# Kernel optimization log

Measured on AMD Instinct MI355X. Metric: run time of the kernel, lower is better.

## Reference

```python
import jax, jax.numpy as jnp
import numpy as np

G = 2            # num_codevector_groups
C = 320          # num_codevectors_per_group
VQ_DIM = 256     # codevector_dim
HID = 512        # conv_dimensions[-1]
TAU = 2.0


def setup_inputs() -> dict:
    key = jax.random.key(0)
    k1, k2, k3, k4 = jax.random.split(key, 4)
    B, S = 16, 2048
    x = jax.random.normal(k1, (B, S, HID), dtype=jnp.float32)
    # iid Gumbel(0,1) noise, same shape as flattened logits [B*S*G, C]
    u = jax.random.uniform(k2, (B * S * G, C), dtype=jnp.float32, minval=1e-6, maxval=1.0 - 1e-6)
    gumbel = -jnp.log(-jnp.log(u))
    Wq = jax.random.normal(k3, (G * C, HID), dtype=jnp.float32) * (1.0 / np.sqrt(HID))
    bq = jnp.zeros((G * C,), dtype=jnp.float32)
    codevectors = jax.random.uniform(k4, (1, G * C, VQ_DIM // G), dtype=jnp.float32)
    return {"x": x, "gumbel": gumbel, "Wq": Wq, "bq": bq, "codevectors": codevectors}


def reference(x, gumbel, Wq, bq, codevectors):
    B, S, H = x.shape
    N = B * S
    logits = jnp.einsum('bsh,gh->bsg', x, Wq) + bq          # [B, S, G*C]
    logits = logits.reshape(N * G, C)

    # hard gumbel-softmax (training path) with straight-through estimator
    y_soft = jax.nn.softmax((logits + gumbel) / TAU, axis=-1)
    idx = jnp.argmax(y_soft, axis=-1)
    y_hard = jax.nn.one_hot(idx, C, dtype=y_soft.dtype)
    probs = y_hard + y_soft - jax.lax.stop_gradient(y_soft)  # [N*G, C]

    # perplexity from plain softmax of logits (no gumbel noise), masked_token_idx=None
    soft_probs = jax.nn.softmax(logits.reshape(N, G, C), axis=-1)
    mean_p = soft_probs.mean(axis=0)                          # [G, C]
    perplexity = jnp.exp(-jnp.sum(mean_p * jnp.log(mean_p + 1e-7), axis=-1)).sum()

    # weighted sum over codes per group == einsum (same math as broadcast*sum in torch)
    cv = codevectors.reshape(G, C, VQ_DIM // G)               # [G, C, d]
    sel = jnp.einsum('ngc,gcd->ngd', probs.reshape(N, G, C), cv)
    selected_codes = sel.reshape(B, S, VQ_DIM)
    return selected_codes, perplexity
```

## Files before the change

### kernel.cpp

```cpp
#include <hip/hip_runtime.h>
#include <hip/hip_fp16.h>

#define HID 512
#define GC  640
#define CC  320
#define GG  2
#define DHALF 128
#define MARGIN 0.004f
#define FB 4

typedef __attribute__((ext_vector_type(8))) _Float16 half8;
typedef __attribute__((ext_vector_type(4))) float float4v;

__device__ __forceinline__ void gload16(const void* g, void* l) {
    __builtin_amdgcn_global_load_lds(
        (const __attribute__((address_space(1))) void*)(unsigned long long)g,
        (__attribute__((address_space(3))) void*)(unsigned)(unsigned long long)l,
        16, 0, 0);
}

__global__ __launch_bounds__(256) void zero_misc(float* meanAcc, int* cnt) {
    for (int i = threadIdx.x; i < GC; i += 256) meanAcc[i] = 0.f;
    if (threadIdx.x < 2) cnt[threadIdx.x] = 0;
}

__global__ __launch_bounds__(256) void convert_f16(
    const float* __restrict__ in, unsigned short* __restrict__ out, int n8)
{
    int i = blockIdx.x * 256 + threadIdx.x;
    if (i >= n8) return;
    const float4* p = (const float4*)in + (size_t)i * 2;
    float4 v0 = p[0], v1 = p[1];
    float f[8] = {v0.x, v0.y, v0.z, v0.w, v1.x, v1.y, v1.z, v1.w};
    unsigned r[4];
#pragma unroll
    for (int j = 0; j < 4; ++j) {
        __half2 hh = __float22half2_rn(make_float2(f[2*j], f[2*j+1]));
        r[j] = __builtin_bit_cast(unsigned, hh);
    }
    uint4 o = {r[0], r[1], r[2], r[3]};
    *(uint4*)(out + (size_t)i * 8) = o;
}

__global__ __launch_bounds__(512, 4) void fused(
    const float* __restrict__ X, const unsigned short* __restrict__ Wh,
    const float* __restrict__ bq, const float* __restrict__ gum,
    const float* __restrict__ cv, float* __restrict__ out,
    float* __restrict__ meanAcc, int* __restrict__ cnt,
    int* __restrict__ flags0, int* __restrict__ flags1)
{
    __shared__ __align__(16) unsigned short As[128 * 32];
    __shared__ __align__(16) unsigned short Bs[384 * 32];
    __shared__ float bqs[CC];
    __shared__ float smean[CC];

    const int tid  = threadIdx.x;
    const int lane = tid & 63;
    const int wid  = tid >> 6;
    const int lq   = lane & 15;
    const int q    = lane >> 4;

    int bid = blockIdx.x;
    int nwg = gridDim.x;
    int swz = ((nwg & 7) == 0) ? (bid & 7) * (nwg >> 3) + (bid >> 3) : bid;
    const int g    = swz & 1;
    const int tok0 = (swz >> 1) * 128;
    int* flagsg = g ? flags1 : flags0;

    for (int i = tid; i < CC; i += 512) { bqs[i] = bq[g * CC + i]; smean[i] = 0.f; }

    float4v acc[20];
#pragma unroll
    for (int j = 0; j < 20; ++j) acc[j] = (float4v){0.f, 0.f, 0.f, 0.f};

    const int arow = tid >> 2, aslot = tid & 3;
    const float* xsrc = X + (size_t)(tok0 + arow) * HID + aslot * 8;

    for (int k0 = 0; k0 < HID; k0 += 32) {
        float4 xa = *(const float4*)(xsrc + k0);
        float4 xb = *(const float4*)(xsrc + k0 + 4);
        half8 h;
        h[0] = (_Float16)xa.x; h[1] = (_Float16)xa.y;
        h[2] = (_Float16)xa.z; h[3] = (_Float16)xa.w;
        h[4] = (_Float16)xb.x; h[5] = (_Float16)xb.y;
        h[6] = (_Float16)xb.z; h[7] = (_Float16)xb.w;
        *(half8*)&As[arow * 32 + aslot * 8] = h;
#pragma unroll
        for (int ii = 0; ii < 3; ++ii) {
            const int iss = wid * 3 + ii;
            int e  = iss * 64 + lane;
            int br = e >> 2; if (br > 319) br = 319;
            int bs = e & 3;
            gload16(Wh + ((size_t)(g * CC + br)) * HID + k0 + bs * 8,
                    &Bs[iss * 512]);
        }
        __syncthreads();
        half8 a = *(const half8*)&As[(wid * 16 + lq) * 32 + q * 8];
#pragma unroll
        for (int j = 0; j < 20; ++j) {
            half8 b = *(const half8*)&Bs[(j * 16 + lq) * 32 + q * 8];
            acc[j] = __builtin_amdgcn_mfma_f32_16x16x32_f16(a, b, acc[j], 0, 0, 0);
        }
        __syncthreads();
    }

    float macc[20];
#pragma unroll
    for (int j = 0; j < 20; ++j) macc[j] = 0.f;

#pragma unroll
    for (int r = 0; r < 4; ++r) {
        const int rowL  = wid * 16 + q * 4 + r;
        const int tglob = tok0 + rowL;
        const float* grow = gum + ((size_t)tglob * GG + g) * CC;
        float le[20];
        float s = 0.f;
        float b = -3.0e38f; int bi = 0; float s2 = -3.0e38f;
#pragma unroll
        for (int j = 0; j < 20; ++j) {
            const int c = j * 16 + lq;
            float lg = acc[j][r] + bqs[c];
            float v  = lg + grow[c];
            if (v > b)       { s2 = b; b = v; bi = c; }
            else if (v > s2) { s2 = v; }
            le[j] = __expf(lg); s += le[j];
        }
#pragma unroll
        for (int m = 1; m < 16; m <<= 1) {
            float os  = __shfl_xor(s,  m, 64);
            float ob  = __shfl_xor(b,  m, 64);
            int   obi = __shfl_xor(bi, m, 64);
            float os2 = __shfl_xor(s2, m, 64);
            s += os;
            if (ob > b || (ob == b && obi < bi)) { s2 = fmaxf(os2, b); b = ob; bi = obi; }
            else                                 { s2 = fmaxf(s2, ob); }
        }
        float inv = 1.f / s;
#pragma unroll
        for (int j = 0; j < 20; ++j) macc[j] += le[j] * inv;

        if (lq == 0 && (b - s2) < MARGIN) {
            int p = atomicAdd(&cnt[g], 1);
            flagsg[p] = tglob;
        }
        const float* cvp = cv + ((size_t)(g * CC + bi)) * DHALF + lq * 8;
        float4 c0v = *(const float4*)cvp;
        float4 c1v = *(const float4*)(cvp + 4);
        float* op = out + (size_t)tglob * 256 + g * DHALF + lq * 8;
        *(float4*)op       = c0v;
        *(float4*)(op + 4) = c1v;
    }
#pragma unroll
    for (int j = 0; j < 20; ++j) {
        macc[j] += __shfl_xor(macc[j], 16, 64);
        macc[j] += __shfl_xor(macc[j], 32, 64);
    }
    if (lane < 16) {
#pragma unroll
        for (int j = 0; j < 20; ++j)
            atomicAdd(&smean[j * 16 + lq], macc[j]);
    }
    __syncthreads();
    for (int i = tid; i < CC; i += 512)
        atomicAdd(&meanAcc[g * CC + i], smean[i]);
}

__global__ __launch_bounds__(320) void fixup(
    const float* __restrict__ X, const float* __restrict__ W,
    const float* __restrict__ bq, const float* __restrict__ gum,
    const float* __restrict__ cv, float* __restrict__ out,
    const int* __restrict__ flags0, const int* __restrict__ flags1,
    const int* __restrict__ cnt)
{
    __shared__ float xs[FB][HID];
    __shared__ float vals[FB][CC];
    __shared__ int stok[FB];
    const int tid = threadIdx.x;
    const int n0 = cnt[0], n1 = cnt[1];
    const int nb0 = (n0 + FB - 1) / FB;
    const int nb1 = (n1 + FB - 1) / FB;

    for (int bb = blockIdx.x; bb < nb0 + nb1; bb += gridDim.x) {
        const int g    = (bb < nb0) ? 0 : 1;
        const int lb   = (bb < nb0) ? bb : bb - nb0;
        const int n    = g ? n1 : n0;
        const int* fl  = g ? flags1 : flags0;
        const int r0   = lb * FB;
        const int nr   = (n - r0 < FB) ? (n - r0) : FB;

        if (tid < FB) {
            int idx = r0 + tid;
            if (idx >= n) idx = n - 1;
            stok[tid] = fl[idx];
        }
        __syncthreads();
        for (int i = tid; i < FB * (HID / 4); i += 320) {
            int r = i >> 7, k4 = i & 127;
            *(float4*)&xs[r][k4 * 4] = *(const float4*)(X + (size_t)stok[r] * HID + k4 * 4);
        }
        __syncthreads();

        {
            const int c = tid;
            if (c < CC) {
                const float* wr = W + (size_t)(g * CC + c) * HID;
                float acc[FB];
#pragma unroll
                for (int r = 0; r < FB; ++r) acc[r] = 0.f;
                for (int k4 = 0; k4 < HID / 4; ++k4) {
                    float4 w4 = *(const float4*)(wr + k4 * 4);
#pragma unroll
                    for (int r = 0; r < FB; ++r) {
                        float4 xv = *(const float4*)&xs[r][k4 * 4];
                        acc[r] = fmaf(xv.x, w4.x, acc[r]);
                        acc[r] = fmaf(xv.y, w4.y, acc[r]);
                        acc[r] = fmaf(xv.z, w4.z, acc[r]);
                        acc[r] = fmaf(xv.w, w4.w, acc[r]);
                    }
                }
                float bias = bq[g * CC + c];
#pragma unroll
                for (int r = 0; r < FB; ++r)
                    vals[r][c] = acc[r] + bias + gum[((size_t)stok[r] * GG + g) * CC + c];
            }
        }
        __syncthreads();

        const int lane = tid & 63;
        const int wv   = tid >> 6;
        if (wv < FB) {
            const int r = wv;
            if (r < nr) {
                float b = -3.0e38f; int bi = 0;
#pragma unroll
                for (int j = 0; j < 5; ++j) {
                    int c = lane + j * 64;
                    float v = vals[r][c];
                    if (v > b || (v == b && c < bi)) { b = v; bi = c; }
                }
#pragma unroll
                for (int m = 32; m; m >>= 1) {
                    float ob = __shfl_xor(b, m, 64);
                    int  obi = __shfl_xor(bi, m, 64);
                    if (ob > b || (ob == b && obi < bi)) { b = ob; bi = obi; }
                }
                int tok = stok[r];
                float2 cvv = *(const float2*)(cv + ((size_t)(g * CC + bi)) * DHALF + lane * 2);
                *(float2*)(out + (size_t)tok * 256 + g * DHALF + lane * 2) = cvv;
            }
        }
        __syncthreads();
    }
}

__global__ __launch_bounds__(256) void perpk(
    const float* __restrict__ meanAcc, float* __restrict__ outp, int ntot)
{
    __shared__ float red0[256];
    __shared__ float red1[256];
    const float invn = 1.f / (float)ntot;
    float h0 = 0.f, h1 = 0.f;
    for (int c = threadIdx.x; c < CC; c += 256) {
        float p0 = meanAcc[c]      * invn;
        float p1 = meanAcc[CC + c] * invn;
        h0 -= p0 * logf(p0 + 1e-7f);
        h1 -= p1 * logf(p1 + 1e-7f);
    }
    red0[threadIdx.x] = h0; red1[threadIdx.x] = h1;
    __syncthreads();
    for (int s = 128; s; s >>= 1) {
        if (threadIdx.x < (unsigned)s) {
            red0[threadIdx.x] += red0[threadIdx.x + s];
            red1[threadIdx.x] += red1[threadIdx.x + s];
        }
        __syncthreads();
    }
    if (threadIdx.x == 0) outp[0] = expf(red0[0]) + expf(red1[0]);
}

extern "C" void kernel_launch(void* const* d_in, const int* in_sizes, int n_in,
                              void* d_out, int out_size, void* d_ws, size_t ws_size,
                              hipStream_t stream) {
    const float* x      = (const float*)d_in[0];
    const float* gumbel = (const float*)d_in[1];
    const float* Wq     = (const float*)d_in[2];
    const float* bq     = (const float*)d_in[3];
    const float* cv     = (const float*)d_in[4];
    float* out = (float*)d_out;

    const int NT = in_sizes[0] / HID;

    char* wsc = (char*)d_ws;
    float* meanAcc = (float*)wsc;
    int*   cnt     = (int*)(wsc + 2560);
    int*   flags0  = (int*)(wsc + 4096);
    int*   flags1  = (int*)(wsc + 135168);
    unsigned short* Wh = (unsigned short*)(wsc + 266240);

    zero_misc<<<1, 256, 0, stream>>>(meanAcc, cnt);
    convert_f16<<<(GC * HID / 8 + 255) / 256, 256, 0, stream>>>(Wq, Wh, GC * HID / 8);

    const int nwg = (NT / 128) * 2;
    fused<<<nwg, 512, 0, stream>>>(x, Wh, bq, gumbel, cv, out,
                                   meanAcc, cnt, flags0, flags1);

    fixup<<<256, 320, 0, stream>>>(x, Wq, bq, gumbel, cv, out, flags0, flags1, cnt);
    perpk<<<1, 256, 0, stream>>>(meanAcc, out + (size_t)out_size - 1, NT);
}
```

Before: 116.8 us.

## Double-buffer weight tiles and load activations directly into MFMA registers

Moves the B (weight) tiles into two LDS buffers so the next k-slice's global-to-LDS loads are issued before the current slice's MFMAs, leaving one barrier per iteration instead of two. It drops the A staging in LDS: each lane loads its own x fragment straight from global memory, prefetched one step ahead, and converts it to half in registers. The B layout becomes k-chunk-major (q*320+row), which removes the padding rows and changes the LDS read pattern. The cost is more LDS (two buffers) and more registers for the prefetched values, which may lower occupancy.

```diff
diff --git a/kernel.cpp b/kernel.cpp
--- a/kernel.cpp
+++ b/kernel.cpp
@@ -49,8 +49,7 @@
     float* __restrict__ meanAcc, int* __restrict__ cnt,
     int* __restrict__ flags0, int* __restrict__ flags1)
 {
-    __shared__ __align__(16) unsigned short As[128 * 32];
-    __shared__ __align__(16) unsigned short Bs[384 * 32];
+    __shared__ __align__(16) unsigned short Bs[2][10240];
     __shared__ float bqs[CC];
     __shared__ float smean[CC];
 
@@ -69,39 +68,53 @@
 
     for (int i = tid; i < CC; i += 512) { bqs[i] = bq[g * CC + i]; smean[i] = 0.f; }
 
+    const int iss0 = wid, iss1 = wid + 8, iss2 = wid + 16;
+    const int m0 = iss0 * 64 + lane, m1 = iss1 * 64 + lane, m2 = iss2 * 64 + lane;
+    const int qc0 = m0 / 320, r0 = m0 - qc0 * 320;
+    const int qc1 = m1 / 320, r1 = m1 - qc1 * 320;
+    const int qc2 = m2 / 320, r2 = m2 - qc2 * 320;
+    const unsigned short* srcB0 = Wh + ((size_t)(g * CC + r0)) * HID + qc0 * 8;
+    const unsigned short* srcB1 = Wh + ((size_t)(g * CC + r1)) * HID + qc1 * 8;
+    const unsigned short* srcB2 = Wh + ((size_t)(g * CC + r2)) * HID + qc2 * 8;
+
+    const float* xsrc = X + (size_t)(tok0 + wid * 16 + lq) * HID + q * 8;
+
     float4v acc[20];
 #pragma unroll
     for (int j = 0; j < 20; ++j) acc[j] = (float4v){0.f, 0.f, 0.f, 0.f};
 
-    const int arow = tid >> 2, aslot = tid & 3;
-    const float* xsrc = X + (size_t)(tok0 + arow) * HID + aslot * 8;
-
-    for (int k0 = 0; k0 < HID; k0 += 32) {
-        float4 xa = *(const float4*)(xsrc + k0);
-        float4 xb = *(const float4*)(xsrc + k0 + 4);
-        half8 h;
-        h[0] = (_Float16)xa.x; h[1] = (_Float16)xa.y;
-        h[2] = (_Float16)xa.z; h[3] = (_Float16)xa.w;
-        h[4] = (_Float16)xb.x; h[5] = (_Float16)xb.y;
-        h[6] = (_Float16)xb.z; h[7] = (_Float16)xb.w;
-        *(half8*)&As[arow * 32 + aslot * 8] = h;
-#pragma unroll
-        for (int ii = 0; ii < 3; ++ii) {
-            const int iss = wid * 3 + ii;
-            int e  = iss * 64 + lane;
-            int br = e >> 2; if (br > 319) br = 319;
-            int bs = e & 3;
-            gload16(Wh + ((size_t)(g * CC + br)) * HID + k0 + bs * 8,
-                    &Bs[iss * 512]);
-        }
-        __syncthreads();
-        half8 a = *(const half8*)&As[(wid * 16 + lq) * 32 + q * 8];
+    gload16(srcB0, &Bs[0][iss0 * 512]);
+    gload16(srcB1, &Bs[0][iss1 * 512]);
+    if (wid < 4) gload16(srcB2, &Bs[0][iss2 * 512]);
+    float4 xa = *(const float4*)xsrc;
+    float4 xb = *(const float4*)(xsrc + 4);
+    __syncthreads();
+
+    int cur = 0;
+    for (int kk = 0; kk < 16; ++kk) {
+        float4 nxa, nxb;
+        if (kk < 15) {
+            const int k0n = (kk + 1) * 32;
+            gload16(srcB0 + k0n, &Bs[cur ^ 1][iss0 * 512]);
+            gload16(srcB1 + k0n, &Bs[cur ^ 1][iss1 * 512]);
+            if (wid < 4) gload16(srcB2 + k0n, &Bs[cur ^ 1][iss2 * 512]);
+            nxa = *(const float4*)(xsrc + k0n);
+            nxb = *(const float4*)(xsrc + k0n + 4);
+        }
+        half8 a;
+        a[0] = (_Float16)xa.x; a[1] = (_Float16)xa.y;
+        a[2] = (_Float16)xa.z; a[3] = (_Float16)xa.w;
+        a[4] = (_Float16)xb.x; a[5] = (_Float16)xb.y;
+        a[6] = (_Float16)xb.z; a[7] = (_Float16)xb.w;
+        const unsigned short* bbase = &Bs[cur][(q * 320 + lq) * 8];
 #pragma unroll
         for (int j = 0; j < 20; ++j) {
-            half8 b = *(const half8*)&Bs[(j * 16 + lq) * 32 + q * 8];
+            half8 b = *(const half8*)(bbase + j * 128);
             acc[j] = __builtin_amdgcn_mfma_f32_16x16x32_f16(a, b, acc[j], 0, 0, 0);
         }
         __syncthreads();
+        if (kk < 15) { xa = nxa; xb = nxb; }
+        cur ^= 1;
     }
 
     float macc[20];
```

New measurement: 157.4 us. 1.35x slower.

## Pre-pack W into MFMA fragment layout and drop LDS staging in GEMM

Applied to the files above, without the earlier changes.

Weights are repacked once into MFMA B-fragment order, so each wave loads its operands straight from global memory (L2) instead of staging A and B through LDS with barriers every k-step. Blocks shrink to 256 threads covering 64 tokens, and each wave converts its own X rows to fp16 in registers. The epilogue transposes logits through an LDS buffer so each lane handles 20 contiguous codes, which gives vectorized float4 gumbel loads. The cost is redundant global/L2 traffic for W, since every wave re-reads the full packed weight slice. Exp is also recomputed in a second pass, and the K loop still carries a leftover __syncthreads per outer step.

```diff
diff --git a/kernel.cpp b/kernel.cpp
--- a/kernel.cpp
+++ b/kernel.cpp
@@ -12,94 +12,80 @@
 typedef __attribute__((ext_vector_type(8))) _Float16 half8;
 typedef __attribute__((ext_vector_type(4))) float float4v;
 
-__device__ __forceinline__ void gload16(const void* g, void* l) {
-    __builtin_amdgcn_global_load_lds(
-        (const __attribute__((address_space(1))) void*)(unsigned long long)g,
-        (__attribute__((address_space(3))) void*)(unsigned)(unsigned long long)l,
-        16, 0, 0);
-}
-
 __global__ __launch_bounds__(256) void zero_misc(float* meanAcc, int* cnt) {
     for (int i = threadIdx.x; i < GC; i += 256) meanAcc[i] = 0.f;
     if (threadIdx.x < 2) cnt[threadIdx.x] = 0;
 }
 
-__global__ __launch_bounds__(256) void convert_f16(
-    const float* __restrict__ in, unsigned short* __restrict__ out, int n8)
+__global__ __launch_bounds__(256) void pack_w(
+    const float* __restrict__ W, unsigned short* __restrict__ Wpk)
 {
-    int i = blockIdx.x * 256 + threadIdx.x;
-    if (i >= n8) return;
-    const float4* p = (const float4*)in + (size_t)i * 2;
-    float4 v0 = p[0], v1 = p[1];
-    float f[8] = {v0.x, v0.y, v0.z, v0.w, v1.x, v1.y, v1.z, v1.w};
-    unsigned r[4];
-#pragma unroll
-    for (int j = 0; j < 4; ++j) {
-        __half2 hh = __float22half2_rn(make_float2(f[2*j], f[2*j+1]));
-        r[j] = __builtin_bit_cast(unsigned, hh);
-    }
-    uint4 o = {r[0], r[1], r[2], r[3]};
-    *(uint4*)(out + (size_t)i * 8) = o;
-}
-
-__global__ __launch_bounds__(512, 4) void fused(
-    const float* __restrict__ X, const unsigned short* __restrict__ Wh,
+    const int t    = blockIdx.x * 4 + (threadIdx.x >> 6);
+    const int lane = threadIdx.x & 63;
+    const int g = t / 320, rem = t % 320, kk = rem / 20, j = rem % 20;
+    const int row = g * 320 + j * 16 + (lane & 15);
+    const int k   = kk * 32 + (lane >> 4) * 8;
+    const float* src = W + (size_t)row * HID + k;
+    float4 xa = *(const float4*)src;
+    float4 xb = *(const float4*)(src + 4);
+    half8 h;
+    h[0] = (_Float16)xa.x; h[1] = (_Float16)xa.y;
+    h[2] = (_Float16)xa.z; h[3] = (_Float16)xa.w;
+    h[4] = (_Float16)xb.x; h[5] = (_Float16)xb.y;
+    h[6] = (_Float16)xb.z; h[7] = (_Float16)xb.w;
+    *(half8*)(Wpk + (size_t)t * 512 + lane * 8) = h;
+}
+
+__global__ __launch_bounds__(256, 4) void fused(
+    const float* __restrict__ X, const unsigned short* __restrict__ Wpk,
     const float* __restrict__ bq, const float* __restrict__ gum,
     const float* __restrict__ cv, float* __restrict__ out,
     float* __restrict__ meanAcc, int* __restrict__ cnt,
     int* __restrict__ flags0, int* __restrict__ flags1)
 {
-    __shared__ __align__(16) unsigned short As[128 * 32];
-    __shared__ __align__(16) unsigned short Bs[384 * 32];
+    __shared__ float rep[4][4][328];
     __shared__ float bqs[CC];
     __shared__ float smean[CC];
 
     const int tid  = threadIdx.x;
     const int lane = tid & 63;
-    const int wid  = tid >> 6;
+    const int wv   = tid >> 6;
     const int lq   = lane & 15;
     const int q    = lane >> 4;
 
-    int bid = blockIdx.x;
-    int nwg = gridDim.x;
+    int bid = blockIdx.x, nwg = gridDim.x;
     int swz = ((nwg & 7) == 0) ? (bid & 7) * (nwg >> 3) + (bid >> 3) : bid;
     const int g    = swz & 1;
-    const int tok0 = (swz >> 1) * 128;
+    const int tok0 = (swz >> 1) * 64 + wv * 16;
     int* flagsg = g ? flags1 : flags0;
 
-    for (int i = tid; i < CC; i += 512) { bqs[i] = bq[g * CC + i]; smean[i] = 0.f; }
+    for (int i = tid; i < CC; i += 256) { bqs[i] = bq[g * CC + i]; smean[i] = 0.f; }
+    __syncthreads();
+
+    const float* xsrc = X + (size_t)(tok0 + lq) * HID + q * 8;
+    const unsigned short* bsrc = Wpk + (size_t)g * 163840 + lane * 8;
 
     float4v acc[20];
 #pragma unroll
     for (int j = 0; j < 20; ++j) acc[j] = (float4v){0.f, 0.f, 0.f, 0.f};
 
-    const int arow = tid >> 2, aslot = tid & 3;
-    const float* xsrc = X + (size_t)(tok0 + arow) * HID + aslot * 8;
-
-    for (int k0 = 0; k0 < HID; k0 += 32) {
-        float4 xa = *(const float4*)(xsrc + k0);
-        float4 xb = *(const float4*)(xsrc + k0 + 4);
-        half8 h;
-        h[0] = (_Float16)xa.x; h[1] = (_Float16)xa.y;
-        h[2] = (_Float16)xa.z; h[3] = (_Float16)xa.w;
-        h[4] = (_Float16)xb.x; h[5] = (_Float16)xb.y;
-        h[6] = (_Float16)xb.z; h[7] = (_Float16)xb.w;
-        *(half8*)&As[arow * 32 + aslot * 8] = h;
-#pragma unroll
-        for (int ii = 0; ii < 3; ++ii) {
-            const int iss = wid * 3 + ii;
-            int e  = iss * 64 + lane;
-            int br = e >> 2; if (br > 319) br = 319;
-            int bs = e & 3;
-            gload16(Wh + ((size_t)(g * CC + br)) * HID + k0 + bs * 8,
-                    &Bs[iss * 512]);
-        }
-        __syncthreads();
-        half8 a = *(const half8*)&As[(wid * 16 + lq) * 32 + q * 8];
-#pragma unroll
-        for (int j = 0; j < 20; ++j) {
-            half8 b = *(const half8*)&Bs[(j * 16 + lq) * 32 + q * 8];
-            acc[j] = __builtin_amdgcn_mfma_f32_16x16x32_f16(a, b, acc[j], 0, 0, 0);
+    for (int ko = 0; ko < 4; ++ko) {
+#pragma unroll
+        for (int ki = 0; ki < 4; ++ki) {
+            const int kk = ko * 4 + ki;
+            float4 xa = *(const float4*)(xsrc + kk * 32);
+            float4 xb = *(const float4*)(xsrc + kk * 32 + 4);
+            half8 a;
+            a[0] = (_Float16)xa.x; a[1] = (_Float16)xa.y;
+            a[2] = (_Float16)xa.z; a[3] = (_Float16)xa.w;
+            a[4] = (_Float16)xb.x; a[5] = (_Float16)xb.y;
+            a[6] = (_Float16)xb.z; a[7] = (_Float16)xb.w;
+            const unsigned short* bk = bsrc + kk * 10240;
+#pragma unroll
+            for (int j = 0; j < 20; ++j) {
+                half8 b = *(const half8*)(bk + j * 512);
+                acc[j] = __builtin_amdgcn_mfma_f32_16x16x32_f16(a, b, acc[j], 0, 0, 0);
+            }
         }
         __syncthreads();
     }
@@ -107,23 +93,33 @@
     float macc[20];
 #pragma unroll
     for (int j = 0; j < 20; ++j) macc[j] = 0.f;
-
-#pragma unroll
+    const int cb = lq * 20;
+
     for (int r = 0; r < 4; ++r) {
-        const int rowL  = wid * 16 + q * 4 + r;
-        const int tglob = tok0 + rowL;
-        const float* grow = gum + ((size_t)tglob * GG + g) * CC;
-        float le[20];
+#pragma unroll
+        for (int j = 0; j < 20; ++j)
+            rep[wv][q][j * 16 + lq] = acc[j][r] + bqs[j * 16 + lq];
+        asm volatile("s_waitcnt lgkmcnt(0)" ::: "memory");
+
+        const int tglob = tok0 + q * 4 + r;
+        const float* rrow = &rep[wv][q][cb];
+        const float* grow = gum + ((size_t)tglob * GG + g) * CC + cb;
+
         float s = 0.f;
         float b = -3.0e38f; int bi = 0; float s2 = -3.0e38f;
 #pragma unroll
-        for (int j = 0; j < 20; ++j) {
-            const int c = j * 16 + lq;
-            float lg = acc[j][r] + bqs[c];
-            float v  = lg + grow[c];
-            if (v > b)       { s2 = b; b = v; bi = c; }
-            else if (v > s2) { s2 = v; }
-            le[j] = __expf(lg); s += le[j];
+        for (int jj = 0; jj < 5; ++jj) {
+            float4 lv = *(const float4*)(rrow + jj * 4);
+            float4 gv = *(const float4*)(grow + jj * 4);
+            float lf[4] = {lv.x, lv.y, lv.z, lv.w};
+            float gf[4] = {gv.x, gv.y, gv.z, gv.w};
+#pragma unroll
+            for (int t = 0; t < 4; ++t) {
+                float v = lf[t] + gf[t];
+                if (v > b)       { s2 = b; b = v; bi = cb + jj * 4 + t; }
+                else if (v > s2) { s2 = v; }
+                s += __expf(lf[t]);
+            }
         }
 #pragma unroll
         for (int m = 1; m < 16; m <<= 1) {
@@ -137,7 +133,13 @@
         }
         float inv = 1.f / s;
 #pragma unroll
-        for (int j = 0; j < 20; ++j) macc[j] += le[j] * inv;
+        for (int jj = 0; jj < 5; ++jj) {
+            float4 lv = *(const float4*)(rrow + jj * 4);
+            macc[jj*4+0] += __expf(lv.x) * inv;
+            macc[jj*4+1] += __expf(lv.y) * inv;
+            macc[jj*4+2] += __expf(lv.z) * inv;
+            macc[jj*4+3] += __expf(lv.w) * inv;
+        }
 
         if (lq == 0 && (b - s2) < MARGIN) {
             int p = atomicAdd(&cnt[g], 1);
@@ -149,7 +151,9 @@
         float* op = out + (size_t)tglob * 256 + g * DHALF + lq * 8;
         *(float4*)op       = c0v;
         *(float4*)(op + 4) = c1v;
-    }
+        asm volatile("s_waitcnt lgkmcnt(0)" ::: "memory");
+    }
+
 #pragma unroll
     for (int j = 0; j < 20; ++j) {
         macc[j] += __shfl_xor(macc[j], 16, 64);
@@ -158,10 +162,10 @@
     if (lane < 16) {
 #pragma unroll
         for (int j = 0; j < 20; ++j)
-            atomicAdd(&smean[j * 16 + lq], macc[j]);
+            atomicAdd(&smean[cb + j], macc[j]);
     }
     __syncthreads();
-    for (int i = tid; i < CC; i += 512)
+    for (int i = tid; i < CC; i += 256)
         atomicAdd(&meanAcc[g * CC + i], smean[i]);
 }
 
@@ -227,9 +231,9 @@
         __syncthreads();
 
         const int lane = tid & 63;
-        const int wv   = tid >> 6;
-        if (wv < FB) {
-            const int r = wv;
+        const int wvv  = tid >> 6;
+        if (wvv < FB) {
+            const int r = wvv;
             if (r < nr) {
                 float b = -3.0e38f; int bi = 0;
 #pragma unroll
@@ -295,13 +299,13 @@
     int*   cnt     = (int*)(wsc + 2560);
     int*   flags0  = (int*)(wsc + 4096);
     int*   flags1  = (int*)(wsc + 135168);
-    unsigned short* Wh = (unsigned short*)(wsc + 266240);
+    unsigned short* Wpk = (unsigned short*)(wsc + 266240);
 
     zero_misc<<<1, 256, 0, stream>>>(meanAcc, cnt);
-    convert_f16<<<(GC * HID / 8 + 255) / 256, 256, 0, stream>>>(Wq, Wh, GC * HID / 8);
-
-    const int nwg = (NT / 128) * 2;
-    fused<<<nwg, 512, 0, stream>>>(x, Wh, bq, gumbel, cv, out,
+    pack_w<<<160, 256, 0, stream>>>(Wq, Wpk);
+
+    const int nwg = (NT / 64) * 2;
+    fused<<<nwg, 256, 0, stream>>>(x, Wpk, bq, gumbel, cv, out,
                                    meanAcc, cnt, flags0, flags1);
 
     fixup<<<256, 320, 0, stream>>>(x, Wq, bq, gumbel, cv, out, flags0, flags1, cnt);
```

Result: slower. 166.9 us (+42.9%).
